# Optimization experiments

Measured on AMD Instinct MI355X. Metric: run time of the kernel, lower is better.

## Reference

```python
import jax, jax.numpy as jnp
import numpy as np

K, N = 4096, 4096
GROUP_SIZE = 64
N_GROUPS = N // GROUP_SIZE
B, S = 4, 2048
NBITS = 4


def setup_inputs() -> dict:
    key = jax.random.key(0)
    ks = jax.random.split(key, 7)
    x = jax.random.normal(ks[0], (B, S, N), dtype=jnp.float32)
    # per-group scales/zeros broadcast over the group_size axis
    scales = jax.random.uniform(ks[1], (K, N_GROUPS, 1), dtype=jnp.float32, minval=0.001, maxval=0.05)
    zeros = jax.random.uniform(ks[2], (K, N_GROUPS, 1), dtype=jnp.float32, minval=0.0, maxval=2.0 ** NBITS - 1)
    mu1 = jax.random.uniform(ks[3], (N,), dtype=jnp.float32, minval=0.5, maxval=1.5)
    mu2 = jax.random.uniform(ks[4], (K,), dtype=jnp.float32, minval=0.5, maxval=1.5)
    bias = jax.random.normal(ks[5], (K,), dtype=jnp.float32)
    W_q = jax.random.randint(ks[6], (K, N), 0, 2 ** NBITS, dtype=jnp.int32)
    return {"x": x, "scales": scales, "zeros": zeros, "mu1": mu1, "mu2": mu2, "bias": bias, "W_q": W_q}


def reference(x, scales, zeros, mu1, mu2, bias, W_q):
    # dequantize: per-group (Q - zero) * scale, then Sinkhorn rescale mu2 (rows) * mu1 (cols)
    k, n = W_q.shape
    n_groups = scales.shape[1]
    Qg = W_q.astype(jnp.float32).reshape(k, n_groups, -1)  # [K, G, gs]
    W_deq = ((Qg - zeros) * scales).reshape(k, n) * mu2[:, None] * mu1[None, :]
    W_deq = W_deq.astype(x.dtype)
    # nn.functional.linear: x @ W^T + b
    return jnp.einsum('bsn,kn->bsk', x, W_deq) + bias
```

## Files before the change

kernel.cpp:

```cpp
#include <hip/hip_runtime.h>
#include <hip/hip_bf16.h>
#include <stdint.h>
#include <type_traits>

typedef unsigned short u16;
typedef __bf16 bf16x8 __attribute__((ext_vector_type(8)));
typedef float f32x4 __attribute__((ext_vector_type(4)));

#define M_TOT 8192
#define N_TOT 4096
#define K_TOT 4096
#define BM 256
#define BN 256
#define BK 64
#define NT 64

#define HALF_EL 8192
#define B_OFF   16384
#define SLOT_EL 32768

template <int V> using ic = std::integral_constant<int, V>;
template <bool V> using bc = std::integral_constant<bool, V>;

__device__ __forceinline__ u16 f2bf(float f) {
    union { float f; uint32_t u; } v; v.f = f;
    uint32_t u = v.u;
    return (u16)((u + 0x7fffu + ((u >> 16) & 1u)) >> 16);
}

__global__ __launch_bounds__(256) void cvt_x_kernel(const float* __restrict__ x,
                                                    u16* __restrict__ xb) {
    const int i = blockIdx.x * blockDim.x + threadIdx.x;
    const float4* p = (const float4*)x + (size_t)i * 2;
    float4 v0 = p[0], v1 = p[1];
    uint4 o;
    o.x = (uint32_t)f2bf(v0.x) | ((uint32_t)f2bf(v0.y) << 16);
    o.y = (uint32_t)f2bf(v0.z) | ((uint32_t)f2bf(v0.w) << 16);
    o.z = (uint32_t)f2bf(v1.x) | ((uint32_t)f2bf(v1.y) << 16);
    o.w = (uint32_t)f2bf(v1.z) | ((uint32_t)f2bf(v1.w) << 16);
    *((uint4*)(xb + (size_t)i * 8)) = o;
}

__global__ __launch_bounds__(256) void deq_w_kernel(const int* __restrict__ wq,
                                                    const float* __restrict__ scales,
                                                    const float* __restrict__ zeros,
                                                    const float* __restrict__ mu1,
                                                    const float* __restrict__ mu2,
                                                    u16* __restrict__ wb) {
    const int i = blockIdx.x * blockDim.x + threadIdx.x;
    const int k  = i >> 9;
    const int n0 = (i & 511) << 3;
    const int g  = n0 >> 6;
    const float z  = zeros[k * 64 + g];
    const float sm = scales[k * 64 + g] * mu2[k];
    const int4* qp = (const int4*)(wq + (size_t)k * N_TOT + n0);
    int4 q0 = qp[0], q1 = qp[1];
    const float4* mp = (const float4*)(mu1 + n0);
    float4 u0 = mp[0], u1 = mp[1];
    uint4 o;
    o.x = (uint32_t)f2bf(((float)q0.x - z) * sm * u0.x) |
          ((uint32_t)f2bf(((float)q0.y - z) * sm * u0.y) << 16);
    o.y = (uint32_t)f2bf(((float)q0.z - z) * sm * u0.z) |
          ((uint32_t)f2bf(((float)q0.w - z) * sm * u0.w) << 16);
    o.z = (uint32_t)f2bf(((float)q1.x - z) * sm * u1.x) |
          ((uint32_t)f2bf(((float)q1.y - z) * sm * u1.y) << 16);
    o.w = (uint32_t)f2bf(((float)q1.z - z) * sm * u1.z) |
          ((uint32_t)f2bf(((float)q1.w - z) * sm * u1.w) << 16);
    *((uint4*)(wb + (size_t)k * N_TOT + n0)) = o;
}

__global__ __launch_bounds__(512, 2) void gemm_kernel(const u16* __restrict__ Xb,
                                                      const u16* __restrict__ Wb,
                                                      const float* __restrict__ bias,
                                                      float* __restrict__ out) {
    __shared__ __align__(16) u16 lds[2 * SLOT_EL];

    const int bid = blockIdx.x;
    const int cpx = gridDim.x >> 3;
    const int swz = (bid & 7) * cpx + (bid >> 3);
    const int bm = swz >> 4;
    const int bn = swz & 15;

    const int tid  = threadIdx.x;
    const int w    = tid >> 6;
    const int lane = tid & 63;
    const int wm = w >> 2, wn = w & 3;

    const int scol = (((lane & 7) ^ (lane >> 3)) << 3);
    const u16* aS = Xb + (size_t)(bm * BM + w * 16 + (lane >> 3)) * N_TOT + scol;
    const u16* bS = Wb + (size_t)(bn * BN + w * 16 + (lane >> 3)) * N_TOT + scol;

    auto stageA = [&](int slot, int h, int u) {
        const u16* s = aS + (size_t)(h * 128) * N_TOT + u * BK;
        u16* d = &lds[slot * SLOT_EL + h * HALF_EL + w * 1024];
        __builtin_amdgcn_global_load_lds(
            (const __attribute__((address_space(1))) uint32_t*)s,
            (__attribute__((address_space(3))) uint32_t*)d, 16, 0, 0);
        __builtin_amdgcn_global_load_lds(
            (const __attribute__((address_space(1))) uint32_t*)(s + (size_t)8 * N_TOT),
            (__attribute__((address_space(3))) uint32_t*)(d + 512), 16, 0, 0);
    };
    auto stageB = [&](int slot, int h, int u) {
        const u16* s = bS + (size_t)(h * 128) * N_TOT + u * BK;
        u16* d = &lds[slot * SLOT_EL + B_OFF + h * HALF_EL + w * 1024];
        __builtin_amdgcn_global_load_lds(
            (const __attribute__((address_space(1))) uint32_t*)s,
            (__attribute__((address_space(3))) uint32_t*)d, 16, 0, 0);
        __builtin_amdgcn_global_load_lds(
            (const __attribute__((address_space(1))) uint32_t*)(s + (size_t)8 * N_TOT),
            (__attribute__((address_space(3))) uint32_t*)(d + 512), 16, 0, 0);
    };

    const int cc0 = (((lane >> 4) << 3)) ^ ((lane & 7) << 3);
    const int rA  = ((wm << 4) + (lane & 15)) << 6;
    const int rB  = ((wn << 4) + (lane & 15)) << 6;

    f32x4 acc[2][2][4][2] = {};
    bf16x8 af[4][2], bf[2][2];

    auto phase = [&](auto Pc, auto Sc, int t) {
        constexpr int P = Pc.value;
        constexpr bool S = Sc.value;
        constexpr int mh = P >> 1, nh = P & 1;
        const int slot = (t & 1) * SLOT_EL;
        if constexpr ((P & 1) == 0) {
            #pragma unroll
            for (int j = 0; j < 4; ++j) {
                af[j][0] = *(const bf16x8*)&lds[slot + mh * HALF_EL + rA + j * 2048 + cc0];
                af[j][1] = *(const bf16x8*)&lds[slot + mh * HALF_EL + rA + j * 2048 + (cc0 ^ 32)];
            }
        }
        #pragma unroll
        for (int j2 = 0; j2 < 2; ++j2) {
            bf[j2][0] = *(const bf16x8*)&lds[slot + B_OFF + nh * HALF_EL + rB + j2 * 4096 + cc0];
            bf[j2][1] = *(const bf16x8*)&lds[slot + B_OFF + nh * HALF_EL + rB + j2 * 4096 + (cc0 ^ 32)];
        }
        if constexpr (S) {
            if constexpr (P == 0) stageA((t + 1) & 1, 1, t + 1);
            if constexpr (P == 1) stageB((t + 1) & 1, 1, t + 1);
            if constexpr (P == 2) stageA(t & 1, 0, t + 2);
            if constexpr (P == 3) stageB(t & 1, 0, t + 2);
        }
        __builtin_amdgcn_s_barrier();
        asm volatile("s_waitcnt lgkmcnt(0)" ::: "memory");
        __builtin_amdgcn_sched_barrier(0);
        __builtin_amdgcn_s_setprio(1);
        #pragma unroll
        for (int j = 0; j < 4; ++j)
            #pragma unroll
            for (int j2 = 0; j2 < 2; ++j2)
                #pragma unroll
                for (int ks = 0; ks < 2; ++ks)
                    acc[mh][nh][j][j2] = __builtin_amdgcn_mfma_f32_16x16x32_bf16(
                        af[j][ks], bf[j2][ks], acc[mh][nh][j][j2], 0, 0, 0);
        __builtin_amdgcn_s_setprio(0);
    };

    auto ktile = [&](auto Mc, auto Vc, int t) {
        constexpr int MASK = Mc.value;
        constexpr int V = Vc.value;
        phase(ic<0>{}, bc<(MASK & 1) != 0>{}, t);
        __builtin_amdgcn_s_barrier();
        phase(ic<1>{}, bc<(MASK & 2) != 0>{}, t);
        __builtin_amdgcn_s_barrier();
        phase(ic<2>{}, bc<(MASK & 4) != 0>{}, t);
        __builtin_amdgcn_s_barrier();
        phase(ic<3>{}, bc<(MASK & 8) != 0>{}, t);
        if constexpr (V == 4) asm volatile("s_waitcnt vmcnt(4)" ::: "memory");
        else if constexpr (V == 0) asm volatile("s_waitcnt vmcnt(0)" ::: "memory");
        __builtin_amdgcn_s_barrier();
    };

    stageA(0, 0, 0); stageB(0, 0, 0); stageA(0, 1, 0); stageB(0, 1, 0);
    stageA(1, 0, 1); stageB(1, 0, 1);
    asm volatile("s_waitcnt vmcnt(4)" ::: "memory");
    __builtin_amdgcn_s_barrier();

    for (int t = 0; t < NT - 2; ++t) ktile(ic<0xF>{}, ic<4>{}, t);
    ktile(ic<0x3>{}, ic<0>{}, NT - 2);
    ktile(ic<0x0>{}, ic<-1>{}, NT - 1);

    #pragma unroll
    for (int mh_ = 0; mh_ < 2; ++mh_)
        #pragma unroll
        for (int j = 0; j < 4; ++j)
            #pragma unroll
            for (int rr = 0; rr < 4; ++rr) {
                const int row = bm * BM + mh_ * 128 + j * 32 + wm * 16 + ((lane >> 4) << 2) + rr;
                float* orow = out + (size_t)row * K_TOT;
                #pragma unroll
                for (int nh_ = 0; nh_ < 2; ++nh_)
                    #pragma unroll
                    for (int j2 = 0; j2 < 2; ++j2) {
                        const int col = bn * BN + nh_ * 128 + j2 * 64 + wn * 16 + (lane & 15);
                        orow[col] = acc[mh_][nh_][j][j2][rr] + bias[col];
                    }
            }
}

extern "C" void kernel_launch(void* const* d_in, const int* in_sizes, int n_in,
                              void* d_out, int out_size, void* d_ws, size_t ws_size,
                              hipStream_t stream) {
    const float* x      = (const float*)d_in[0];
    const float* scales = (const float*)d_in[1];
    const float* zeros  = (const float*)d_in[2];
    const float* mu1    = (const float*)d_in[3];
    const float* mu2    = (const float*)d_in[4];
    const float* bias   = (const float*)d_in[5];
    const int*   wq     = (const int*)d_in[6];
    float* out = (float*)d_out;

    u16* xb = (u16*)d_ws;
    u16* wb = (u16*)d_ws + (size_t)M_TOT * N_TOT;

    cvt_x_kernel<<<(M_TOT * N_TOT / 8) / 256, 256, 0, stream>>>(x, xb);
    deq_w_kernel<<<(K_TOT * N_TOT / 8) / 256, 256, 0, stream>>>(wq, scales, zeros, mu1, mu2, wb);
    gemm_kernel<<<(M_TOT / BM) * (K_TOT / BN), 512, 0, stream>>>(xb, wb, bias, out);
}
```

Before: 287.1 us.

## Keep A and B fragments in registers across phases and restructure prefetch schedule

Each k-tile now loads both A halves and both B halves into registers during phases 0 and 1 and reuses them in phases 2 and 3. The B half is no longer reloaded from LDS in every phase. The prefetch schedule changes from a two-tiles-ahead split-slot scheme to prefetching the whole next tile into the alternate slot across the four phases, with vmcnt waits per phase. This cuts LDS read traffic and the prologue stage, but raises register pressure from doubled fragment arrays and shortens the lead time of global loads.

```diff
diff --git a/kernel.cpp b/kernel.cpp
--- a/kernel.cpp
+++ b/kernel.cpp
@@ -116,30 +116,32 @@
     const int rB  = ((wn << 4) + (lane & 15)) << 6;
 
     f32x4 acc[2][2][4][2] = {};
-    bf16x8 af[4][2], bf[2][2];
-
-    auto phase = [&](auto Pc, auto Sc, int t) {
+    bf16x8 af[2][4][2];
+    bf16x8 bf[2][2][2];
+
+    auto phase = [&](auto Pc, auto Sc, auto Wc, int t) {
         constexpr int P = Pc.value;
         constexpr bool S = Sc.value;
+        constexpr int W = Wc.value;
         constexpr int mh = P >> 1, nh = P & 1;
         const int slot = (t & 1) * SLOT_EL;
-        if constexpr ((P & 1) == 0) {
+        if constexpr (P == 0 || P == 1) {
             #pragma unroll
             for (int j = 0; j < 4; ++j) {
-                af[j][0] = *(const bf16x8*)&lds[slot + mh * HALF_EL + rA + j * 2048 + cc0];
-                af[j][1] = *(const bf16x8*)&lds[slot + mh * HALF_EL + rA + j * 2048 + (cc0 ^ 32)];
+                af[P][j][0] = *(const bf16x8*)&lds[slot + P * HALF_EL + rA + j * 2048 + cc0];
+                af[P][j][1] = *(const bf16x8*)&lds[slot + P * HALF_EL + rA + j * 2048 + (cc0 ^ 32)];
+            }
+            #pragma unroll
+            for (int j2 = 0; j2 < 2; ++j2) {
+                bf[P][j2][0] = *(const bf16x8*)&lds[slot + B_OFF + P * HALF_EL + rB + j2 * 4096 + cc0];
+                bf[P][j2][1] = *(const bf16x8*)&lds[slot + B_OFF + P * HALF_EL + rB + j2 * 4096 + (cc0 ^ 32)];
             }
         }
-        #pragma unroll
-        for (int j2 = 0; j2 < 2; ++j2) {
-            bf[j2][0] = *(const bf16x8*)&lds[slot + B_OFF + nh * HALF_EL + rB + j2 * 4096 + cc0];
-            bf[j2][1] = *(const bf16x8*)&lds[slot + B_OFF + nh * HALF_EL + rB + j2 * 4096 + (cc0 ^ 32)];
-        }
         if constexpr (S) {
-            if constexpr (P == 0) stageA((t + 1) & 1, 1, t + 1);
-            if constexpr (P == 1) stageB((t + 1) & 1, 1, t + 1);
-            if constexpr (P == 2) stageA(t & 1, 0, t + 2);
-            if constexpr (P == 3) stageB(t & 1, 0, t + 2);
+            if constexpr (P == 0) stageA((t + 1) & 1, 0, t + 1);
+            if constexpr (P == 1) stageB((t + 1) & 1, 0, t + 1);
+            if constexpr (P == 2) stageA((t + 1) & 1, 1, t + 1);
+            if constexpr (P == 3) stageB((t + 1) & 1, 1, t + 1);
         }
         __builtin_amdgcn_s_barrier();
         asm volatile("s_waitcnt lgkmcnt(0)" ::: "memory");
@@ -152,33 +154,28 @@
                 #pragma unroll
                 for (int ks = 0; ks < 2; ++ks)
                     acc[mh][nh][j][j2] = __builtin_amdgcn_mfma_f32_16x16x32_bf16(
-                        af[j][ks], bf[j2][ks], acc[mh][nh][j][j2], 0, 0, 0);
+                        af[mh][j][ks], bf[nh][j2][ks], acc[mh][nh][j][j2], 0, 0, 0);
         __builtin_amdgcn_s_setprio(0);
-    };
-
-    auto ktile = [&](auto Mc, auto Vc, int t) {
-        constexpr int MASK = Mc.value;
-        constexpr int V = Vc.value;
-        phase(ic<0>{}, bc<(MASK & 1) != 0>{}, t);
-        __builtin_amdgcn_s_barrier();
-        phase(ic<1>{}, bc<(MASK & 2) != 0>{}, t);
-        __builtin_amdgcn_s_barrier();
-        phase(ic<2>{}, bc<(MASK & 4) != 0>{}, t);
-        __builtin_amdgcn_s_barrier();
-        phase(ic<3>{}, bc<(MASK & 8) != 0>{}, t);
-        if constexpr (V == 4) asm volatile("s_waitcnt vmcnt(4)" ::: "memory");
-        else if constexpr (V == 0) asm volatile("s_waitcnt vmcnt(0)" ::: "memory");
+        if constexpr (W == 0)      asm volatile("s_waitcnt vmcnt(0)" ::: "memory");
+        else if constexpr (W == 2) asm volatile("s_waitcnt vmcnt(2)" ::: "memory");
+        else if constexpr (W == 4) asm volatile("s_waitcnt vmcnt(4)" ::: "memory");
         __builtin_amdgcn_s_barrier();
     };
 
     stageA(0, 0, 0); stageB(0, 0, 0); stageA(0, 1, 0); stageB(0, 1, 0);
-    stageA(1, 0, 1); stageB(1, 0, 1);
     asm volatile("s_waitcnt vmcnt(4)" ::: "memory");
     __builtin_amdgcn_s_barrier();
 
-    for (int t = 0; t < NT - 2; ++t) ktile(ic<0xF>{}, ic<4>{}, t);
-    ktile(ic<0x3>{}, ic<0>{}, NT - 2);
-    ktile(ic<0x0>{}, ic<-1>{}, NT - 1);
+    for (int t = 0; t < NT - 1; ++t) {
+        phase(ic<0>{}, bc<true>{}, ic<2>{}, t);
+        phase(ic<1>{}, bc<true>{}, ic<-1>{}, t);
+        phase(ic<2>{}, bc<true>{}, ic<-1>{}, t);
+        phase(ic<3>{}, bc<true>{}, ic<4>{}, t);
+    }
+    phase(ic<0>{}, bc<false>{}, ic<0>{}, NT - 1);
+    phase(ic<1>{}, bc<false>{}, ic<-1>{}, NT - 1);
+    phase(ic<2>{}, bc<false>{}, ic<-1>{}, NT - 1);
+    phase(ic<3>{}, bc<false>{}, ic<-1>{}, NT - 1);
 
     #pragma unroll
     for (int mh_ = 0; mh_ < 2; ++mh_)
```

Result: faster. 280.4 us (-2.3%).
